# Kernel tuning notes

Hardware: AMD Instinct MI355X
Metric: run time of the kernel (lower is better)

## Reference

```python
import jax, jax.numpy as jnp
import numpy as np

N_EMBED = 1024
HEAD_SIZE = 128
B, T = 8, 2048

def setup_inputs() -> dict:
    key = jax.random.key(0)
    kx, kq, kk, kv = jax.random.split(key, 4)
    x = jax.random.normal(kx, (B, T, N_EMBED), dtype=jnp.float32)
    s = N_EMBED ** -0.5
    Wq = jax.random.normal(kq, (N_EMBED, HEAD_SIZE), dtype=jnp.float32) * s
    Wk = jax.random.normal(kk, (N_EMBED, HEAD_SIZE), dtype=jnp.float32) * s
    Wv = jax.random.normal(kv, (N_EMBED, HEAD_SIZE), dtype=jnp.float32) * s
    return {"x": x, "Wq": Wq, "Wk": Wk, "Wv": Wv}

def reference(x, Wq, Wk, Wv):
    # x: [B, T, C]; single causal attention head, eval mode (dropout = identity).
    Bb, Tt, C = x.shape
    q = x @ Wq  # [B, T, H]
    k = x @ Wk  # [B, T, H]
    v = x @ Wv  # [B, T, H]
    # NOTE: original scales by C**-0.5 with C = n_embed (input dim), not head_size.
    wgt = jnp.einsum('bqh,bkh->bqk', q, k) * (C ** -0.5)  # [B, T, T]
    causal = jnp.tril(jnp.ones((Tt, Tt), dtype=bool))
    wgt = jnp.where(causal, wgt, -jnp.inf)
    wgt = jax.nn.softmax(wgt, axis=-1)
    return wgt @ v  # [B, T, H]
```

## Files before the change

### kernel.cpp

```cpp
#include <hip/hip_runtime.h>
#include <hip/hip_bf16.h>

#define B_  8
#define T_  2048
#define C_  1024
#define H_  128

using f32x4  = __attribute__((ext_vector_type(4))) float;
using bf16x8 = __attribute__((ext_vector_type(8))) short;

__device__ __forceinline__ unsigned short f2bf(float f) {
    union { float f; unsigned u; } v; v.f = f;
    unsigned r = v.u + 0x7FFFu + ((v.u >> 16) & 1u);
    return (unsigned short)(r >> 16);
}

template<int C>
__device__ __forceinline__ float dppf(float v) {
    return __int_as_float(__builtin_amdgcn_update_dpp(0, __float_as_int(v), C, 0xF, 0xF, true));
}
#define DPPRED_MAX(v) { v = fmaxf(v, dppf<0xB1>(v)); v = fmaxf(v, dppf<0x4E>(v)); \
                        v = fmaxf(v, dppf<0x141>(v)); v = fmaxf(v, dppf<0x140>(v)); }
#define DPPRED_SUM(v) { v = v + dppf<0xB1>(v); v = v + dppf<0x4E>(v); \
                        v = v + dppf<0x141>(v); v = v + dppf<0x140>(v); }

__global__ void wconv_kernel(const float* __restrict__ Wq,
                             const float* __restrict__ Wk,
                             const float* __restrict__ Wv,
                             unsigned short* __restrict__ Wt) {
    int id  = blockIdx.x * 256 + threadIdx.x;
    int col = id % 384;
    int k   = id / 384;
    const float* W = (col < 128) ? Wq : ((col < 256) ? Wk : Wv);
    float v = W[k * H_ + (col & 127)];
    if (col < 128) v *= 0.03125f;
    Wt[(size_t)(k >> 5) * 12288 + col * 32 + (k & 31)] = f2bf(v);
}

__launch_bounds__(256, 2)
__global__ void gemm_kernel(const float* __restrict__ x,
                            const unsigned short* __restrict__ Wt,
                            unsigned short* __restrict__ qb,
                            unsigned short* __restrict__ kb,
                            unsigned short* __restrict__ vT) {
    __shared__ unsigned short Bs[2][12288];
    __shared__ unsigned short As[2][32][32];

    const int tid  = threadIdx.x;
    const int wave = tid >> 6;
    const int lane = tid & 63;
    const int lo = lane & 15, hi = lane >> 4;
    const int row0  = blockIdx.x * 32;
    const int col0w = wave * 96;

    const int srow = tid >> 3;
    const int sk4  = (tid & 7) * 4;
    const float* xsrc = x + (size_t)(row0 + srow) * C_ + sk4;

    f32x4 acc[2][6];
    #pragma unroll
    for (int rt = 0; rt < 2; ++rt)
        #pragma unroll
        for (int ct = 0; ct < 6; ++ct)
            acc[rt][ct] = f32x4{0.f, 0.f, 0.f, 0.f};

    {
        const unsigned short* bsrc = Wt + (size_t)tid * 8;
        #pragma unroll
        for (int j = 0; j < 6; ++j)
            *(uint4*)&Bs[0][tid * 8 + j * 2048] = *(const uint4*)(bsrc + j * 2048);
        float4 f = *(const float4*)(xsrc);
        unsigned a0 = f2bf(f.x) | ((unsigned)f2bf(f.y) << 16);
        unsigned a1 = f2bf(f.z) | ((unsigned)f2bf(f.w) << 16);
        *(uint2*)&As[0][srow][sk4] = uint2{a0, a1};
    }
    __syncthreads();

    for (int k = 0; k < 32; ++k) {
        const int cur = k & 1;

        uint4 br[6];
        float4 xf;
        if (k < 31) {
            const unsigned short* bsrc = Wt + (size_t)(k + 1) * 12288 + tid * 8;
            #pragma unroll
            for (int j = 0; j < 6; ++j)
                br[j] = *(const uint4*)(bsrc + j * 2048);
            xf = *(const float4*)(xsrc + (k + 1) * 32);
        }

        bf16x8 af[2], bfr[6];
        #pragma unroll
        for (int rt = 0; rt < 2; ++rt)
            af[rt] = *(const bf16x8*)&As[cur][rt * 16 + lo][hi * 8];
        #pragma unroll
        for (int ct = 0; ct < 6; ++ct)
            bfr[ct] = *(const bf16x8*)&Bs[cur][(col0w + ct * 16 + lo) * 32 + hi * 8];

        __builtin_amdgcn_s_setprio(1);
        #pragma unroll
        for (int ct = 0; ct < 6; ++ct)
            #pragma unroll
            for (int rt = 0; rt < 2; ++rt)
                acc[rt][ct] = __builtin_amdgcn_mfma_f32_16x16x32_bf16(af[rt], bfr[ct], acc[rt][ct], 0, 0, 0);
        __builtin_amdgcn_s_setprio(0);

        if (k < 31) {
            #pragma unroll
            for (int j = 0; j < 6; ++j)
                *(uint4*)&Bs[cur ^ 1][tid * 8 + j * 2048] = br[j];
            unsigned a0 = f2bf(xf.x) | ((unsigned)f2bf(xf.y) << 16);
            unsigned a1 = f2bf(xf.z) | ((unsigned)f2bf(xf.w) << 16);
            *(uint2*)&As[cur ^ 1][srow][sk4] = uint2{a0, a1};
        }
        __syncthreads();
    }

    #pragma unroll
    for (int ct = 0; ct < 6; ++ct) {
        int col = col0w + ct * 16 + lo;
        int head = col >> 7;
        int h = col & 127;
        #pragma unroll
        for (int rt = 0; rt < 2; ++rt) {
            #pragma unroll
            for (int r = 0; r < 4; ++r) {
                int rg = row0 + rt * 16 + 4 * hi + r;
                unsigned short val = f2bf(acc[rt][ct][r]);
                if (head == 0)      qb[(size_t)rg * H_ + h] = val;
                else if (head == 1) kb[(size_t)rg * H_ + h] = val;
                else {
                    int b = rg >> 11, t = rg & (T_ - 1);
                    vT[((size_t)b * H_ + h) * T_ + t] = val;
                }
            }
        }
    }
}

__launch_bounds__(512, 2)
__global__ void attn1_kernel(const unsigned short* __restrict__ qb,
                             const unsigned short* __restrict__ kb,
                             const unsigned short* __restrict__ vT,
                             float* __restrict__ Opart,
                             float* __restrict__ MLpart) {
    __shared__ unsigned short Ks[64 * 128];
    __shared__ unsigned short Vs[128 * 64];
    __shared__ unsigned short Ps[8][16][72];

    const int tid  = threadIdx.x;
    const int wave = tid >> 6;
    const int lane = tid & 63;
    const int lo = lane & 15, hi = lane >> 4;

    const int bid   = blockIdx.x;
    const int b     = bid & 7;
    const int chunk = (bid >> 3) & 7;
    const int qt    = 7 - (bid >> 6);
    if (chunk > qt) return;

    const int kv_begin = chunk << 8;
    const size_t bT = (size_t)b * T_;
    const int qrow0 = (qt << 8) + wave * 32;

    const int krow = tid >> 3, kcol = (tid & 7) * 2;
    const int vrow = tid >> 2, vcol = (tid & 3) * 2;
    const unsigned short* kgsrc = kb + (bT + krow) * H_ + kcol * 8;
    const unsigned short* vgsrc = vT + ((size_t)b * H_ + vrow) * T_ + vcol * 8;
    unsigned short* kdst0 = &Ks[krow * 128 + ((kcol ^ (krow & 7)) * 8)];
    unsigned short* kdst1 = &Ks[krow * 128 + (((kcol + 1) ^ (krow & 7)) * 8)];
    unsigned short* vdst0 = &Vs[vrow * 64 + ((vcol ^ (vrow & 7)) * 8)];
    unsigned short* vdst1 = &Vs[vrow * 64 + (((vcol + 1) ^ (vrow & 7)) * 8)];

    bf16x8 qf[2][4];
    #pragma unroll
    for (int q2 = 0; q2 < 2; ++q2)
        #pragma unroll
        for (int kc = 0; kc < 4; ++kc)
            qf[q2][kc] = *(const bf16x8*)(qb + (bT + qrow0 + 16 * q2 + lo) * H_ + kc * 32 + 8 * hi);

    float m[2][4], l[2][4];
    f32x4 o[2][8];
    #pragma unroll
    for (int q2 = 0; q2 < 2; ++q2)
        #pragma unroll
        for (int r = 0; r < 4; ++r) { m[q2][r] = -1e30f; l[q2][r] = 0.f; }
    #pragma unroll
    for (int q2 = 0; q2 < 2; ++q2)
        #pragma unroll
        for (int ct = 0; ct < 8; ++ct) o[q2][ct] = f32x4{0.f, 0.f, 0.f, 0.f};

    uint4 kr0 = *(const uint4*)(kgsrc + (size_t)kv_begin * H_);
    uint4 kr1 = *(const uint4*)(kgsrc + (size_t)kv_begin * H_ + 8);
    uint4 vr0 = *(const uint4*)(vgsrc + kv_begin);
    uint4 vr1 = *(const uint4*)(vgsrc + kv_begin + 8);

    for (int t = 0; t < 4; ++t) {
        const int kv0 = kv_begin + t * 64;
        __syncthreads();
        *(uint4*)kdst0 = kr0;
        *(uint4*)kdst1 = kr1;
        *(uint4*)vdst0 = vr0;
        *(uint4*)vdst1 = vr1;
        __syncthreads();
        if (t < 3) {
            const int kvn = kv0 + 64;
            kr0 = *(const uint4*)(kgsrc + (size_t)kvn * H_);
            kr1 = *(const uint4*)(kgsrc + (size_t)kvn * H_ + 8);
            vr0 = *(const uint4*)(vgsrc + kvn);
            vr1 = *(const uint4*)(vgsrc + kvn + 8);
        }
        if (kv0 > qrow0 + 31) continue;

        f32x4 s[2][4];
        #pragma unroll
        for (int q2 = 0; q2 < 2; ++q2)
            #pragma unroll
            for (int ct4 = 0; ct4 < 4; ++ct4) s[q2][ct4] = f32x4{0.f, 0.f, 0.f, 0.f};
        __builtin_amdgcn_s_setprio(1);
        #pragma unroll
        for (int ct4 = 0; ct4 < 4; ++ct4) {
            const int row = ct4 * 16 + lo;
            #pragma unroll
            for (int kc = 0; kc < 4; ++kc) {
                bf16x8 kf = *(const bf16x8*)&Ks[row * 128 + (((kc * 4 + hi) ^ (row & 7)) * 8)];
                s[0][ct4] = __builtin_amdgcn_mfma_f32_16x16x32_bf16(qf[0][kc], kf, s[0][ct4], 0, 0, 0);
                s[1][ct4] = __builtin_amdgcn_mfma_f32_16x16x32_bf16(qf[1][kc], kf, s[1][ct4], 0, 0, 0);
            }
        }
        __builtin_amdgcn_s_setprio(0);

        if (kv0 + 63 >= qrow0) {
            #pragma unroll
            for (int q2 = 0; q2 < 2; ++q2)
                #pragma unroll
                for (int ct4 = 0; ct4 < 4; ++ct4)
                    #pragma unroll
                    for (int r = 0; r < 4; ++r)
                        if (kv0 + ct4 * 16 + lo > qrow0 + 16 * q2 + 4 * hi + r)
                            s[q2][ct4][r] = -1e30f;
        }

        float alpha[2][4];
        #pragma unroll
        for (int q2 = 0; q2 < 2; ++q2) {
            #pragma unroll
            for (int r = 0; r < 4; ++r) {
                float pm = fmaxf(fmaxf(s[q2][0][r], s[q2][1][r]), fmaxf(s[q2][2][r], s[q2][3][r]));
                DPPRED_MAX(pm);
                float mn = fmaxf(m[q2][r], pm);
                alpha[q2][r] = __expf(m[q2][r] - mn);
                m[q2][r] = mn;
                #pragma unroll
                for (int ct4 = 0; ct4 < 4; ++ct4) s[q2][ct4][r] = __expf(s[q2][ct4][r] - mn);
                float rs = (s[q2][0][r] + s[q2][1][r]) + (s[q2][2][r] + s[q2][3][r]);
                DPPRED_SUM(rs);
                l[q2][r] = l[q2][r] * alpha[q2][r] + rs;
            }
        }
        #pragma unroll
        for (int q2 = 0; q2 < 2; ++q2)
            #pragma unroll
            for (int ct = 0; ct < 8; ++ct)
                #pragma unroll
                for (int r = 0; r < 4; ++r) o[q2][ct][r] *= alpha[q2][r];

        bf16x8 pa[2][2];
        #pragma unroll
        for (int q2 = 0; q2 < 2; ++q2) {
            #pragma unroll
            for (int ct4 = 0; ct4 < 4; ++ct4)
                #pragma unroll
                for (int r = 0; r < 4; ++r)
                    Ps[wave][4 * hi + r][ct4 * 16 + lo] = f2bf(s[q2][ct4][r]);
            pa[q2][0] = *(const bf16x8*)&Ps[wave][lo][8 * hi];
            pa[q2][1] = *(const bf16x8*)&Ps[wave][lo][32 + 8 * hi];
        }

        __builtin_amdgcn_s_setprio(1);
        #pragma unroll
        for (int ct = 0; ct < 8; ++ct) {
            const int row = ct * 16 + lo;
            #pragma unroll
            for (int half = 0; half < 2; ++half) {
                bf16x8 vf = *(const bf16x8*)&Vs[row * 64 + (((half * 4 + hi) ^ (row & 7)) * 8)];
                o[0][ct] = __builtin_amdgcn_mfma_f32_16x16x32_bf16(pa[0][half], vf, o[0][ct], 0, 0, 0);
                o[1][ct] = __builtin_amdgcn_mfma_f32_16x16x32_bf16(pa[1][half], vf, o[1][ct], 0, 0, 0);
            }
        }
        __builtin_amdgcn_s_setprio(0);
    }

    const int slot = b * 36 + ((qt * (qt + 1)) >> 1) + chunk;
    float* op = Opart + (size_t)slot * 32768 + (size_t)(wave * 32) * 128;
    #pragma unroll
    for (int q2 = 0; q2 < 2; ++q2)
        #pragma unroll
        for (int ct = 0; ct < 8; ++ct)
            #pragma unroll
            for (int r = 0; r < 4; ++r)
                op[(16 * q2 + 4 * hi + r) * 128 + ct * 16 + lo] = o[q2][ct][r];
    if (lo == 0) {
        #pragma unroll
        for (int q2 = 0; q2 < 2; ++q2)
            #pragma unroll
            for (int r = 0; r < 4; ++r) {
                int base = slot * 512 + (wave * 32 + 16 * q2 + 4 * hi + r) * 2;
                MLpart[base]     = m[q2][r];
                MLpart[base + 1] = l[q2][r];
            }
    }
}

__launch_bounds__(128)
__global__ void attn2_kernel(const float* __restrict__ Opart,
                             const float* __restrict__ MLpart,
                             float* __restrict__ out) {
    const int bid = blockIdx.x;
    const int b   = bid & 7;
    const int qt  = (bid >> 3) & 7;
    const int sub = bid >> 6;
    const int nch = qt + 1;
    const int slot0 = b * 36 + ((qt * (qt + 1)) >> 1);

    const int tid  = threadIdx.x;
    const int row  = tid >> 2;
    const int h0   = (tid & 3) * 32;
    const int srow = sub * 32 + row;

    float M = -1e30f;
    for (int c = 0; c < nch; ++c)
        M = fmaxf(M, MLpart[(slot0 + c) * 512 + srow * 2]);
    float L = 0.f;
    for (int c = 0; c < nch; ++c) {
        float mc = MLpart[(slot0 + c) * 512 + srow * 2];
        float lc = MLpart[(slot0 + c) * 512 + srow * 2 + 1];
        L += lc * __expf(mc - M);
    }

    float4 acc[8];
    #pragma unroll
    for (int j = 0; j < 8; ++j) acc[j] = float4{0.f, 0.f, 0.f, 0.f};
    for (int c = 0; c < nch; ++c) {
        float wc = __expf(MLpart[(slot0 + c) * 512 + srow * 2] - M);
        const float4* src = (const float4*)(Opart + (size_t)(slot0 + c) * 32768 + (size_t)srow * 128 + h0);
        #pragma unroll
        for (int j = 0; j < 8; ++j) {
            float4 v = src[j];
            acc[j].x += wc * v.x; acc[j].y += wc * v.y;
            acc[j].z += wc * v.z; acc[j].w += wc * v.w;
        }
    }
    float inv = 1.f / L;
    float4* dst = (float4*)(out + ((size_t)b * T_ + qt * 256 + srow) * H_ + h0);
    #pragma unroll
    for (int j = 0; j < 8; ++j) {
        float4 v = acc[j];
        dst[j] = float4{v.x * inv, v.y * inv, v.z * inv, v.w * inv};
    }
}

extern "C" void kernel_launch(void* const* d_in, const int* in_sizes, int n_in,
                              void* d_out, int out_size, void* d_ws, size_t ws_size,
                              hipStream_t stream) {
    const float* x  = (const float*)d_in[0];
    const float* Wq = (const float*)d_in[1];
    const float* Wk = (const float*)d_in[2];
    const float* Wv = (const float*)d_in[3];
    float* out = (float*)d_out;

    char* ws = (char*)d_ws;
    unsigned short* Wt  = (unsigned short*)ws;
    unsigned short* qbf = (unsigned short*)(ws + (size_t)384 * 1024 * 2);
    unsigned short* kbf = qbf + (size_t)B_ * T_ * H_;
    unsigned short* vTf = kbf + (size_t)B_ * T_ * H_;
    float* Opart  = (float*)(vTf + (size_t)B_ * T_ * H_);
    float* MLpart = (float*)((char*)Opart + (size_t)288 * 32768 * 4);

    wconv_kernel<<<(384 * 1024) / 256, 256, 0, stream>>>(Wq, Wk, Wv, Wt);
    gemm_kernel<<<B_ * T_ / 32, 256, 0, stream>>>(x, Wt, qbf, kbf, vTf);
    attn1_kernel<<<512, 512, 0, stream>>>(qbf, kbf, vTf, Opart, MLpart);
    attn2_kernel<<<512, 128, 0, stream>>>(Opart, MLpart, out);
}
```

Baseline: 88.84 us.

## Deepen GEMM global prefetch to two stages and use lighter LDS-only barriers

The projection GEMM now keeps two K-tiles of weights and x in registers, issuing global loads two iterations ahead instead of one, so load latency is hidden across more MFMA work. The __syncthreads calls in both the GEMM and attention loops are replaced by a barrier that waits only on LDS counters (lgkmcnt) rather than all outstanding memory, so in-flight global prefetches no longer stall at the barrier. The setprio hints around the MFMA block are dropped. This raises register pressure (another 6 uint4 plus a float4 per thread) and adds redundant reloads of the last tile at the tail.

New measurement: 252.9 us. 2.85x slower.

```diff
diff --git a/kernel.cpp b/kernel.cpp
--- a/kernel.cpp
+++ b/kernel.cpp
@@ -14,6 +14,9 @@
     unsigned r = v.u + 0x7FFFu + ((v.u >> 16) & 1u);
     return (unsigned short)(r >> 16);
 }
+
+#define BAR() do { asm volatile("s_waitcnt lgkmcnt(0)" ::: "memory"); \
+                   __builtin_amdgcn_s_barrier(); } while (0)
 
 template<int C>
 __device__ __forceinline__ float dppf(float v) {
@@ -56,6 +59,7 @@
     const int srow = tid >> 3;
     const int sk4  = (tid & 7) * 4;
     const float* xsrc = x + (size_t)(row0 + srow) * C_ + sk4;
+    const unsigned short* bsrc = Wt + tid * 8;
 
     f32x4 acc[2][6];
     #pragma unroll
@@ -65,7 +69,6 @@
             acc[rt][ct] = f32x4{0.f, 0.f, 0.f, 0.f};
 
     {
-        const unsigned short* bsrc = Wt + (size_t)tid * 8;
         #pragma unroll
         for (int j = 0; j < 6; ++j)
             *(uint4*)&Bs[0][tid * 8 + j * 2048] = *(const uint4*)(bsrc + j * 2048);
@@ -74,20 +77,20 @@
         unsigned a1 = f2bf(f.z) | ((unsigned)f2bf(f.w) << 16);
         *(uint2*)&As[0][srow][sk4] = uint2{a0, a1};
     }
-    __syncthreads();
+    uint4 brA[6], brB[6];
+    float4 hA, hB;
+    #pragma unroll
+    for (int j = 0; j < 6; ++j)
+        brA[j] = *(const uint4*)(bsrc + 12288 + j * 2048);
+    hA = *(const float4*)(xsrc + 32);
+    #pragma unroll
+    for (int j = 0; j < 6; ++j)
+        brB[j] = *(const uint4*)(bsrc + 2 * 12288 + j * 2048);
+    hB = *(const float4*)(xsrc + 64);
+    BAR();
 
     for (int k = 0; k < 32; ++k) {
-        const int cur = k & 1;
-
-        uint4 br[6];
-        float4 xf;
-        if (k < 31) {
-            const unsigned short* bsrc = Wt + (size_t)(k + 1) * 12288 + tid * 8;
-            #pragma unroll
-            for (int j = 0; j < 6; ++j)
-                br[j] = *(const uint4*)(bsrc + j * 2048);
-            xf = *(const float4*)(xsrc + (k + 1) * 32);
-        }
+        const int cur = k & 1, nxt = cur ^ 1;
 
         bf16x8 af[2], bfr[6];
         #pragma unroll
@@ -97,23 +100,34 @@
         for (int ct = 0; ct < 6; ++ct)
             bfr[ct] = *(const bf16x8*)&Bs[cur][(col0w + ct * 16 + lo) * 32 + hi * 8];
 
-        __builtin_amdgcn_s_setprio(1);
         #pragma unroll
         for (int ct = 0; ct < 6; ++ct)
             #pragma unroll
             for (int rt = 0; rt < 2; ++rt)
                 acc[rt][ct] = __builtin_amdgcn_mfma_f32_16x16x32_bf16(af[rt], bfr[ct], acc[rt][ct], 0, 0, 0);
-        __builtin_amdgcn_s_setprio(0);
 
         if (k < 31) {
             #pragma unroll
             for (int j = 0; j < 6; ++j)
-                *(uint4*)&Bs[cur ^ 1][tid * 8 + j * 2048] = br[j];
-            unsigned a0 = f2bf(xf.x) | ((unsigned)f2bf(xf.y) << 16);
-            unsigned a1 = f2bf(xf.z) | ((unsigned)f2bf(xf.w) << 16);
-            *(uint2*)&As[cur ^ 1][srow][sk4] = uint2{a0, a1};
-        }
-        __syncthreads();
+                *(uint4*)&Bs[nxt][tid * 8 + j * 2048] = brA[j];
+            unsigned a0 = f2bf(hA.x) | ((unsigned)f2bf(hA.y) << 16);
+            unsigned a1 = f2bf(hA.z) | ((unsigned)f2bf(hA.w) << 16);
+            *(uint2*)&As[nxt][srow][sk4] = uint2{a0, a1};
+        }
+
+        #pragma unroll
+        for (int j = 0; j < 6; ++j) brA[j] = brB[j];
+        hA = hB;
+        {
+            const int kn = (k + 3 < 31) ? k + 3 : 31;
+            const unsigned short* g = bsrc + (size_t)kn * 12288;
+            #pragma unroll
+            for (int j = 0; j < 6; ++j)
+                brB[j] = *(const uint4*)(g + j * 2048);
+            hB = *(const float4*)(xsrc + kn * 32);
+        }
+
+        BAR();
     }
 
     #pragma unroll
@@ -197,12 +211,12 @@
 
     for (int t = 0; t < 4; ++t) {
         const int kv0 = kv_begin + t * 64;
-        __syncthreads();
+        BAR();
         *(uint4*)kdst0 = kr0;
         *(uint4*)kdst1 = kr1;
         *(uint4*)vdst0 = vr0;
         *(uint4*)vdst1 = vr1;
-        __syncthreads();
+        BAR();
         if (t < 3) {
             const int kvn = kv0 + 64;
             kr0 = *(const uint4*)(kgsrc + (size_t)kvn * H_);
```
